# Performance work log

Measured on AMD Instinct MI355X. Metric: run time of the kernel, lower is better.

Reference implementation:

```python
import jax, jax.numpy as jnp
import numpy as np

B, V, K = 4, 16384, 16
E, F, D, H, L, ITERS = 32, 2, 64, 4, 2, 10
NEG = -1e9


def setup_inputs() -> dict:
    key = jax.random.key(0)
    ks = jax.random.split(key, 24)
    def g(k, shape, fan_in):
        return jax.random.normal(k, shape, dtype=jnp.float32) * (fan_in ** -0.5)
    inp = {}
    inp["node_embeddings"] = jax.random.normal(ks[0], (B, V, E), dtype=jnp.float32)
    inp["node_features"] = jax.random.normal(ks[1], (B, V, F), dtype=jnp.float32)
    inp["demands"] = jax.random.normal(ks[2], (B, V, 1), dtype=jnp.float32)
    # padded adjacency list; value == V means masked (no neighbor)
    inp["adj_lst"] = jax.random.randint(ks[3], (B, V, K), 0, V + 1, dtype=jnp.int32)
    # precomputed inverse-adjacency indices; reference computes inflow by scatter-add instead
    inp["flow_indices"] = jax.random.randint(ks[4], (B, V, K), 0, V, dtype=jnp.int32)
    inp["num_nodes"] = V
    din = E + F
    inp["W_enc1"] = g(ks[5], (din, D), din); inp["b_enc1"] = jnp.zeros((D,), jnp.float32)
    inp["W_enc2"] = g(ks[6], (D, D), D); inp["b_enc2"] = jnp.zeros((D,), jnp.float32)
    inp["W_gat"] = g(ks[7], (H, D, D), D)
    inp["a_src"] = g(ks[8], (H, D), D)
    inp["a_dst"] = g(ks[9], (H, D), D)
    for i, nm in enumerate(["z", "r", "c"]):
        inp["W_" + nm] = g(ks[10 + 2 * i], (D, D), D)
        inp["U_" + nm] = g(ks[11 + 2 * i], (D, D), D)
        inp["b_" + nm] = jnp.zeros((D,), jnp.float32)
    inp["W_dec1"] = g(ks[16], (D, D), D); inp["b_dec1"] = jnp.zeros((D,), jnp.float32)
    inp["W_dec2"] = g(ks[17], (D, 1), D); inp["b_dec2"] = jnp.zeros((1,), jnp.float32)
    return inp


def _forward(node_embeddings, node_features, demands,
             W_enc1, b_enc1, W_enc2, b_enc2,
             W_gat, a_src, a_dst,
             W_z, U_z, b_z, W_r, U_r, b_r, W_c, U_c, b_c,
             W_dec1, b_dec1, W_dec2, b_dec2,
             adj_lst, num_nodes):
    Vn = num_nodes
    bidx = jnp.arange(adj_lst.shape[0])[:, None, None]  # [B,1,1]
    mask = adj_lst == Vn  # [B,V,K] padded slots

    # --- node encoder MLP (tanh, activate_final=True) ---
    x = jnp.concatenate([node_embeddings, node_features], axis=-1)
    h = jnp.tanh(x @ W_enc1 + b_enc1)
    h = jnp.tanh(h @ W_enc2 + b_enc2)

    def gather_nodes(t):
        # masked_gather: pad with a zero row so index == num_nodes reads zeros
        t_pad = jnp.concatenate([t, jnp.zeros_like(t[:, :1])], axis=1)  # [B,V+1,Dt]
        return t_pad[bidx, adj_lst]  # [B,V,K,Dt]

    # --- graph_layers x (AdjGAT + GRU) ---
    for _ in range(L):
        agg = 0.0
        for hd in range(H):
            t = h @ W_gat[hd]                       # [B,V,D]
            nb = gather_nodes(t)                    # [B,V,K,D]
            scores = (t @ a_src[hd])[:, :, None] + nb @ a_dst[hd]  # [B,V,K]
            attn = jax.nn.softmax(jnp.where(mask, NEG, scores), axis=-1)
            agg = agg + jnp.einsum('bvk,bvkd->bvd', attn, nb)
        m = jnp.tanh(agg / H)
        z = jax.nn.sigmoid(m @ W_z + h @ U_z + b_z)
        r = jax.nn.sigmoid(m @ W_r + h @ U_r + b_r)
        c = jnp.tanh(m @ W_c + (r * h) @ U_c + b_c)
        h = (1.0 - z) * h + z * c

    # --- decoder -> per-edge weights via masked gather + softmax ---
    node_w = jnp.tanh(h @ W_dec1 + b_dec1) @ W_dec2 + b_dec2   # [B,V,1]
    pw = gather_nodes(node_w)[..., 0]                          # [B,V,K]
    norm_w = jax.nn.softmax(jnp.where(mask, NEG, pw), axis=-1)

    # --- iterative min-cost-flow solver ---
    flow0 = norm_w * jax.nn.relu(-demands)  # sources (demand<0) push supply
    def body(carry, _):
        flow, _ = carry
        inflow = jnp.zeros((flow.shape[0], Vn + 1), flow.dtype)
        inflow = inflow.at[bidx, adj_lst].add(flow)[:, :Vn]    # [B,V]
        new = norm_w * jax.nn.relu(inflow[..., None] - demands)
        return (new, flow), None
    (flow, pflow), _ = jax.lax.scan(body, (flow0, flow0), None, length=ITERS)

    flow_cost = jnp.sum(flow * flow, axis=(1, 2))  # quadratic cost_fn
    return flow, flow_cost, norm_w, pflow


def reference(node_embeddings, node_features, demands, adj_lst, flow_indices, num_nodes,
              W_enc1, b_enc1, W_enc2, b_enc2, W_gat, a_src, a_dst,
              W_z, U_z, b_z, W_r, U_r, b_r, W_c, U_c, b_c,
              W_dec1, b_dec1, W_dec2, b_dec2):
    # flow_indices is the precomputed inverse adjacency; inflow is computed
    # equivalently here by scatter-add over adj_lst.
    return _forward(node_embeddings, node_features, demands,
                    W_enc1, b_enc1, W_enc2, b_enc2,
                    W_gat, a_src, a_dst,
                    W_z, U_z, b_z, W_r, U_r, b_r, W_c, U_c, b_c,
                    W_dec1, b_dec1, W_dec2, b_dec2,
                    adj_lst, num_nodes)
```

## Files before the change

kernel.cpp:

```cpp
#include <hip/hip_runtime.h>
#include <stdint.h>
#include <math.h>

#define BN 4
#define VN 16384
#define KN 16
#define HN 4
#define NN (BN*VN)
#define EN (VN*KN)
#define CAP 64
#define NEGC (-1.0e9f)

typedef __attribute__((ext_vector_type(8))) short short8;
typedef __attribute__((ext_vector_type(4))) float floatx4;
typedef __attribute__((ext_vector_type(2))) float floatx2;
typedef unsigned short u16;
typedef unsigned int u32;

#define OFF_H      0ull
#define OFF_M      8388608ull
#define OFF_T      16777216ull
#define OFF_SS     50331648ull
#define OFF_NW     52428800ull
#define OFF_NV     52690944ull
#define OFF_CNT    53215232ull
#define OFF_PG     53477376ull
#define OFF_PZR    (OFF_PG  + 32768ull)
#define OFF_PC     (OFF_PZR + 32768ull)
#define OFF_PE1    (OFF_PC  + 16384ull)
#define OFF_PE2    (OFF_PE1 + 8192ull)
#define OFF_PD1    (OFF_PE2 + 8192ull)
#define OFF_PAV    (OFF_PD1 + 8192ull)

__device__ __forceinline__ u16 f2bf(float x){
  union { float f; unsigned int u; } c; c.f = x;
  unsigned int r = c.u + 0x7fffu + ((c.u >> 16) & 1u);
  return (u16)(r >> 16);
}
__device__ __forceinline__ float bf2f(u32 s){
  union { unsigned int u; float f; } c; c.u = s << 16;
  return c.f;
}
__device__ __forceinline__ float sigm(float x){ return 1.0f/(1.0f+expf(-x)); }

union S8 { short8 v; u16 u[8]; };

__global__ __launch_bounds__(256) void k_pack(
    const float* __restrict__ Wg,  const float* __restrict__ Wz, const float* __restrict__ Uz,
    const float* __restrict__ Wr,  const float* __restrict__ Ur, const float* __restrict__ Wc,
    const float* __restrict__ Uc,  const float* __restrict__ We1, const float* __restrict__ We2,
    const float* __restrict__ Wd1, const float* __restrict__ asrc, const float* __restrict__ adst,
    u16* __restrict__ pg, u16* __restrict__ pzr, u16* __restrict__ pc,
    u16* __restrict__ pe1, u16* __restrict__ pe2, u16* __restrict__ pd1,
    u16* __restrict__ pav)
{
  int e = blockIdx.x*256 + threadIdx.x;
  if (e >= 54272) return;
  int el; u16* dst; int CN; int region;
  if      (e < 16384){ el = e;        dst = pg;  CN = 2; region = 0; }
  else if (e < 32768){ el = e-16384;  dst = pzr; CN = 4; region = 1; }
  else if (e < 40960){ el = e-32768;  dst = pc;  CN = 4; region = 2; }
  else if (e < 45056){ el = e-40960;  dst = pe1; CN = 2; region = 3; }
  else if (e < 49152){ el = e-45056;  dst = pe2; CN = 2; region = 4; }
  else if (e < 53248){ el = e-49152;  dst = pd1; CN = 2; region = 5; }
  else               { el = e-53248;  dst = pav; CN = 2; region = 6; }
  int j    = el & 7;
  int lane = (el >> 3) & 63;
  int rest = el >> 9;
  int c  = rest % CN;
  int ng = rest / CN;
  int k  = c*32 + (lane>>4)*8 + j;
  int n  = ng*16 + (lane&15);
  float val = 0.0f;
  if (region == 0){
    val = Wg[(size_t)(n>>6)*4096 + k*64 + (n&63)];
  } else if (region == 1){
    int km = (k&3)*16 + ((k>>2)&15);
    if (n < 64) val = (k<64) ? Wz[km*64+n]      : Uz[(k-64)*64+n];
    else        val = (k<64) ? Wr[km*64+(n-64)] : Ur[(k-64)*64+(n-64)];
  } else if (region == 2){
    int km = (k&3)*16 + ((k>>2)&15);
    val = (k<64) ? Wc[km*64+n] : Uc[(k-64)*64+n];
  } else if (region == 3){
    val = (k<34) ? We1[k*64+n] : 0.0f;
  } else if (region == 4){
    val = We2[k*64+n];
  } else if (region == 5){
    val = Wd1[k*64+n];
  } else {
    int hd = (n>>1)&3, s = n&1;
    const float* av = s ? (adst + hd*64) : (asrc + hd*64);
    const float* wrow = Wg + (size_t)hd*4096 + k*64;
    float acc = 0.f;
    #pragma unroll 8
    for (int d=0; d<64; d++) acc += wrow[d]*av[d];
    val = acc;
  }
  dst[el] = f2bf(val);
}

template<int CN>
__device__ __forceinline__ void load_b(const u16* p, int chunk, int lane, short8 Bf[CN][4]){
  const short8* P = (const short8*)p;
  #pragma unroll
  for (int c=0;c<CN;c++)
    #pragma unroll
    for (int ng=0; ng<4; ng++)
      Bf[c][ng] = P[((chunk*4+ng)*CN + c)*64 + lane];
}

template<int CN>
__device__ __forceinline__ void mfma_tile(const short8* A, const short8 Bf[CN][4],
                                          floatx4 acc[4][4], int wave, int lane){
  #pragma unroll
  for (int c=0;c<CN;c++){
    #pragma unroll
    for (int mg=0;mg<4;mg++){
      short8 a = A[((wave*4+mg)*CN + c)*64 + lane];
      #pragma unroll
      for (int ng=0;ng<4;ng++)
        acc[mg][ng] = __builtin_amdgcn_mfma_f32_16x16x32_bf16(a, Bf[c][ng], acc[mg][ng], 0, 0, 0);
    }
  }
}

__device__ __forceinline__ void zero_acc(floatx4 acc[4][4]){
  #pragma unroll
  for (int mg=0;mg<4;mg++)
    #pragma unroll
    for (int ng=0;ng<4;ng++){
      floatx4 z = {0.f,0.f,0.f,0.f};
      acc[mg][ng] = z;
    }
}

__global__ __launch_bounds__(128) void k_enc(
    const float* __restrict__ emb, const float* __restrict__ feat,
    const u16* __restrict__ pe1, const u16* __restrict__ pe2,
    const float* __restrict__ be1, const float* __restrict__ be2,
    u16* __restrict__ hout, u32* __restrict__ cnt)
{
  cnt[blockIdx.x*128 + threadIdx.x] = 0u;
  __shared__ short8 A1[1024];
  __shared__ short8 A2[1024];
  const int tid = threadIdx.x;
  const int n0  = blockIdx.x * 128;
  for (int it=0; it<8; ++it){
    int slot = it*128 + tid;
    int row = slot >> 3, jc = slot & 7;
    S8 w;
    if (jc < 4){
      const float* s = emb + (size_t)(n0+row)*32 + jc*8;
      #pragma unroll
      for (int j=0;j<8;j++) w.u[j] = f2bf(s[j]);
    } else if (jc == 4){
      const float* s = feat + (size_t)(n0+row)*2;
      w.u[0] = f2bf(s[0]); w.u[1] = f2bf(s[1]);
      #pragma unroll
      for (int j=2;j<8;j++) w.u[j] = 0;
    } else {
      #pragma unroll
      for (int j=0;j<8;j++) w.u[j] = 0;
    }
    A1[((row>>4)*2 + (jc>>2))*64 + (jc&3)*16 + (row&15)] = w.v;
  }
  __syncthreads();
  const int wave = tid>>6, lane = tid&63, q = lane>>4, ml = lane&15;

  short8 Bf[2][4];
  load_b<2>(pe1, 0, lane, Bf);
  floatx4 acc[4][4];
  zero_acc(acc);
  mfma_tile<2>(A1, Bf, acc, wave, lane);

  u16* A2s = (u16*)A2;
  #pragma unroll
  for (int mg=0;mg<4;mg++){
    #pragma unroll
    for (int r=0;r<4;r++){
      int row_l = wave*64 + mg*16 + q*4 + r;
      #pragma unroll
      for (int ng=0;ng<4;ng++){
        int k2 = ng*16 + ml;
        float v = tanhf(acc[mg][ng][r] + be1[k2]);
        int c2 = k2>>5, q2=(k2>>3)&3, j2=k2&7;
        A2s[ (((row_l>>4)*2 + c2)*64 + q2*16 + (row_l&15))*8 + j2 ] = f2bf(v);
      }
    }
  }
  __syncthreads();

  load_b<2>(pe2, 0, lane, Bf);
  zero_acc(acc);
  mfma_tile<2>(A2, Bf, acc, wave, lane);
  #pragma unroll
  for (int mg=0;mg<4;mg++)
    #pragma unroll
    for (int r=0;r<4;r++){
      int row = n0 + wave*64 + mg*16 + q*4 + r;
      #pragma unroll
      for (int ng=0;ng<4;ng++){
        int col = ng*16 + ml;
        hout[(size_t)row*64 + col] = f2bf(tanhf(acc[mg][ng][r] + be2[col]));
      }
    }
}

__global__ __launch_bounds__(128) void k_t(
    const u16* __restrict__ h, const u16* __restrict__ pg, const u16* __restrict__ pav,
    u32* __restrict__ tq, float* __restrict__ ss)
{
  __shared__ short8 A[1024];
  const int tid = threadIdx.x;
  const int n0  = blockIdx.x * 128;
  const short8* hp = (const short8*)h;
  for (int it=0; it<8; ++it){
    int slot = it*128 + tid;
    int row = slot >> 3, jc = slot & 7;
    A[((row>>4)*2 + (jc>>2))*64 + (jc&3)*16 + (row&15)] = hp[(size_t)(n0+row)*8 + jc];
  }
  __syncthreads();
  const int wave = tid>>6, lane = tid&63, q = lane>>4, ml = lane&15;

  for (int chunk=0; chunk<4; ++chunk){
    short8 Bf[2][4];
    load_b<2>(pg, chunk, lane, Bf);
    floatx4 acc[4][4];
    zero_acc(acc);
    mfma_tile<2>(A, Bf, acc, wave, lane);

    #pragma unroll
    for (int mg=0;mg<4;mg++){
      #pragma unroll
      for (int r=0;r<4;r++){
        int row = n0 + wave*64 + mg*16 + q*4 + r;
        int pk = __builtin_amdgcn_cvt_pk_fp8_f32(acc[mg][0][r], acc[mg][1][r], 0, false);
        pk     = __builtin_amdgcn_cvt_pk_fp8_f32(acc[mg][2][r], acc[mg][3][r], pk, true);
        tq[(size_t)row*64 + chunk*16 + ml] = (u32)pk;
      }
    }
  }

  const short8* Pv = (const short8*)pav;
  short8 Bs0 = Pv[lane], Bs1 = Pv[64 + lane];
  #pragma unroll
  for (int mg=0;mg<4;mg++){
    floatx4 sacc = {0.f,0.f,0.f,0.f};
    short8 a0 = A[((wave*4+mg)*2 + 0)*64 + lane];
    short8 a1 = A[((wave*4+mg)*2 + 1)*64 + lane];
    sacc = __builtin_amdgcn_mfma_f32_16x16x32_bf16(a0, Bs0, sacc, 0, 0, 0);
    sacc = __builtin_amdgcn_mfma_f32_16x16x32_bf16(a1, Bs1, sacc, 0, 0, 0);
    if (ml < 8){
      #pragma unroll
      for (int r=0;r<4;r++){
        int row = n0 + wave*64 + mg*16 + q*4 + r;
        ss[(size_t)row*8 + ml] = sacc[r];
      }
    }
  }
}

__global__ __launch_bounds__(256) void k_attn(
    const int* __restrict__ adj, const u32* __restrict__ tq,
    const float* __restrict__ ss, u16* __restrict__ m)
{
  const int wave = threadIdx.x>>6, lane = threadIdx.x&63;
  const int nid = blockIdx.x*4 + wave;
  const int b = nid >> 14;
  const int hd = lane>>4;
  int u = adj[(size_t)nid*16 + (lane&15)];
  float sc = (u == VN) ? NEGC : (ss[(size_t)nid*8 + hd*2] + ss[((size_t)b*VN + u)*8 + hd*2 + 1]);
  float mx = sc;
  #pragma unroll
  for (int s=1;s<16;s<<=1) mx = fmaxf(mx, __shfl_xor(mx, s, 64));
  float ex = expf(sc - mx);
  float sm = ex;
  #pragma unroll
  for (int s=1;s<16;s<<=1) sm += __shfl_xor(sm, s, 64);
  float attn = ex / sm;

  float a0=0.f, a1=0.f, a2=0.f, a3=0.f;
  const int srcl = lane & 48;
  #pragma unroll
  for (int k2=0;k2<16;k2++){
    int u2 = __shfl(u, k2, 64);
    float av = __shfl(attn, srcl + k2, 64);
    u32 w = tq[((size_t)b*VN + u2)*64 + lane];
    floatx2 f01 = __builtin_amdgcn_cvt_pk_f32_fp8((int)w, false);
    floatx2 f23 = __builtin_amdgcn_cvt_pk_f32_fp8((int)w, true);
    a0 += av*f01.x; a1 += av*f01.y; a2 += av*f23.x; a3 += av*f23.y;
  }
  a0 += __shfl_xor(a0,16,64); a0 += __shfl_xor(a0,32,64);
  a1 += __shfl_xor(a1,16,64); a1 += __shfl_xor(a1,32,64);
  a2 += __shfl_xor(a2,16,64); a2 += __shfl_xor(a2,32,64);
  a3 += __shfl_xor(a3,16,64); a3 += __shfl_xor(a3,32,64);
  if (lane < 16){
    union { uint2 v; u16 u[4]; } val;
    val.u[0] = f2bf(tanhf(a0*0.25f)); val.u[1] = f2bf(tanhf(a1*0.25f));
    val.u[2] = f2bf(tanhf(a2*0.25f)); val.u[3] = f2bf(tanhf(a3*0.25f));
    *(uint2*)(m + (size_t)nid*64 + lane*4) = val.v;
  }
}

__global__ __launch_bounds__(128) void k_gru(
    const u16* __restrict__ m, u16* __restrict__ h,
    const u16* __restrict__ pzr, const u16* __restrict__ pc_,
    const float* __restrict__ bz, const float* __restrict__ br,
    const float* __restrict__ bc_)
{
  __shared__ short8 A[2048];
  const int tid = threadIdx.x;
  const int n0  = blockIdx.x * 128;
  const short8* mp = (const short8*)m;
  const short8* hp = (const short8*)h;
  for (int it=0; it<16; ++it){
    int slot = it*128 + tid;
    int row = slot >> 4, jc = slot & 15;
    short8 w = (jc < 8) ? mp[(size_t)(n0+row)*8 + jc]
                        : hp[(size_t)(n0+row)*8 + (jc-8)];
    A[((row>>4)*4 + (jc>>2))*64 + (jc&3)*16 + (row&15)] = w;
  }
  __syncthreads();
  const int wave = tid>>6, lane = tid&63, q = lane>>4, ml = lane&15;

  short8 Bf[4][4];

  floatx4 zacc[4][4];
  load_b<4>(pzr, 0, lane, Bf);
  zero_acc(zacc);
  mfma_tile<4>(A, Bf, zacc, wave, lane);

  floatx4 acc[4][4];
  load_b<4>(pzr, 1, lane, Bf);
  zero_acc(acc);
  mfma_tile<4>(A, Bf, acc, wave, lane);

  floatx4 h_old[4][4];
  u16* As = (u16*)A;
  #pragma unroll
  for (int mg=0;mg<4;mg++){
    #pragma unroll
    for (int r=0;r<4;r++){
      int row_l = wave*64 + mg*16 + q*4 + r;
      int row   = n0 + row_l;
      #pragma unroll
      for (int ng=0;ng<4;ng++){
        int col = ng*16 + ml;
        float rv = sigm(acc[mg][ng][r] + br[col]);
        float hv = bf2f(h[(size_t)row*64 + col]);
        h_old[mg][ng][r] = hv;
        int kk = 64 + col;
        int c2 = kk>>5, q2 = (kk>>3)&3, j2 = kk&7;
        As[ (((row_l>>4)*4 + c2)*64 + q2*16 + (row_l&15))*8 + j2 ] = f2bf(hv*rv);
      }
    }
  }

  load_b<4>(pc_, 0, lane, Bf);
  zero_acc(acc);
  mfma_tile<4>(A, Bf, acc, wave, lane);

  #pragma unroll
  for (int mg=0;mg<4;mg++)
    #pragma unroll
    for (int r=0;r<4;r++){
      int row = n0 + wave*64 + mg*16 + q*4 + r;
      #pragma unroll
      for (int ng=0;ng<4;ng++){
        int col = ng*16 + ml;
        float zv = sigm(zacc[mg][ng][r] + bz[col]);
        float cv = tanhf(acc[mg][ng][r] + bc_[col]);
        float ho = h_old[mg][ng][r];
        h[(size_t)row*64 + col] = f2bf((1.f - zv)*ho + zv*cv);
      }
    }
}

__global__ __launch_bounds__(128) void k_dec(
    const u16* __restrict__ h, const u16* __restrict__ pd1,
    const float* __restrict__ bd1, const float* __restrict__ Wd2, const float* __restrict__ bd2,
    float* __restrict__ nodew, float* __restrict__ cost)
{
  {
    int t = blockIdx.x*128 + threadIdx.x;
    if (t < BN) cost[t] = 0.f;
  }
  __shared__ short8 A[1024];
  const int tid = threadIdx.x;
  const int n0  = blockIdx.x * 128;
  const short8* hp = (const short8*)h;
  for (int it=0; it<8; ++it){
    int slot = it*128 + tid;
    int row = slot >> 3, jc = slot & 7;
    A[((row>>4)*2 + (jc>>2))*64 + (jc&3)*16 + (row&15)] = hp[(size_t)(n0+row)*8 + jc];
  }
  __syncthreads();
  const int wave = tid>>6, lane = tid&63, q = lane>>4, ml = lane&15;

  short8 Bf[2][4];
  load_b<2>(pd1, 0, lane, Bf);
  floatx4 acc[4][4];
  zero_acc(acc);
  mfma_tile<2>(A, Bf, acc, wave, lane);

  float wd2l[4];
  #pragma unroll
  for (int ng=0;ng<4;ng++) wd2l[ng] = Wd2[ng*16 + ml];
  float b2 = bd2[0];
  #pragma unroll
  for (int mg=0;mg<4;mg++)
    #pragma unroll
    for (int r=0;r<4;r++){
      int row = n0 + wave*64 + mg*16 + q*4 + r;
      float ps = 0.f;
      #pragma unroll
      for (int ng=0;ng<4;ng++)
        ps += tanhf(acc[mg][ng][r] + bd1[ng*16+ml]) * wd2l[ng];
      #pragma unroll
      for (int s=1;s<16;s<<=1) ps += __shfl_xor(ps, s, 64);
      if (ml == 0) nodew[row] = ps + b2;
    }
}

__global__ __launch_bounds__(256) void k_pw(
    const int* __restrict__ adj, const float* __restrict__ nodew, const float* __restrict__ dem,
    float* __restrict__ normw, float* __restrict__ nv0,
    u32* __restrict__ cnt, u32* __restrict__ bucket)
{
  int e = blockIdx.x*256 + threadIdx.x;
  int node = e >> 4;
  int b = node >> 14;
  int u = adj[e];
  float pw = (u == VN) ? NEGC : nodew[(size_t)b*VN + u];
  float mx = pw;
  #pragma unroll
  for (int s=1;s<16;s<<=1) mx = fmaxf(mx, __shfl_xor(mx, s, 64));
  float ex = expf(pw - mx);
  float sm = ex;
  #pragma unroll
  for (int s=1;s<16;s<<=1) sm += __shfl_xor(sm, s, 64);
  float nw = ex / sm;
  normw[e] = nw;
  if ((e & 15) == 0) nv0[node] = fmaxf(-dem[node], 0.f);
  if (u < VN){
    int g = b*VN + u;
    u32 pos = atomicAdd(&cnt[g], 1u);
    if (pos < CAP)
      bucket[(size_t)g*CAP + pos] = ((u32)f2bf(nw) << 16) | (u32)(node & (VN-1));
  }
}

__global__ __launch_bounds__(256) void k_gather(
    const u32* __restrict__ cnt, const u32* __restrict__ bucket,
    const float* __restrict__ dem, const float* __restrict__ nvin, float* __restrict__ nvout,
    const float* __restrict__ normw, float* __restrict__ fout, float* __restrict__ cost)
{
  int tid = blockIdx.x*256 + threadIdx.x;
  int g = tid >> 4;
  int lane = tid & 15;
  int b = g >> 14;
  u32 n = cnt[g];
  if (n > CAP) n = CAP;
  const u32* bk = bucket + (size_t)g*CAP;
  const float* nb = nvin + (size_t)b*VN;
  float sum = 0.f;
  for (u32 i = (u32)lane; i < n; i += 16u){
    u32 r = bk[i];
    sum += bf2f(r >> 16) * nb[r & 0xFFFFu];
  }
  #pragma unroll
  for (int sh=1; sh<16; sh<<=1) sum += __shfl_xor(sum, sh, 64);
  float nvv = fmaxf(sum - dem[g], 0.f);
  if (lane == 0) nvout[g] = nvv;
  if (fout){
    int e = g*16 + lane;
    float fl = normw[e] * nvv;
    fout[e] = fl;
    if (cost){
      float ssq = fl*fl;
      #pragma unroll
      for (int sh=1; sh<64; sh<<=1) ssq += __shfl_xor(ssq, sh, 64);
      __shared__ float part[4];
      if ((threadIdx.x & 63) == 0) part[threadIdx.x>>6] = ssq;
      __syncthreads();
      if (threadIdx.x == 0) atomicAdd(cost + b, part[0]+part[1]+part[2]+part[3]);
    }
  }
}

extern "C" void kernel_launch(void* const* d_in, const int* in_sizes, int n_in,
                              void* d_out, int out_size, void* d_ws, size_t ws_size,
                              hipStream_t stream)
{
  const float* emb  = (const float*)d_in[0];
  const float* feat = (const float*)d_in[1];
  const float* dem  = (const float*)d_in[2];
  const int*   adj  = (const int*)  d_in[3];
  const float* We1 = (const float*)d_in[6];
  const float* be1 = (const float*)d_in[7];
  const float* We2 = (const float*)d_in[8];
  const float* be2 = (const float*)d_in[9];
  const float* Wg  = (const float*)d_in[10];
  const float* asrc= (const float*)d_in[11];
  const float* adst= (const float*)d_in[12];
  const float* Wz  = (const float*)d_in[13];
  const float* Uz  = (const float*)d_in[14];
  const float* bz  = (const float*)d_in[15];
  const float* Wr  = (const float*)d_in[16];
  const float* Ur  = (const float*)d_in[17];
  const float* br  = (const float*)d_in[18];
  const float* Wc  = (const float*)d_in[19];
  const float* Uc  = (const float*)d_in[20];
  const float* bc  = (const float*)d_in[21];
  const float* Wd1 = (const float*)d_in[22];
  const float* bd1 = (const float*)d_in[23];
  const float* Wd2 = (const float*)d_in[24];
  const float* bd2 = (const float*)d_in[25];

  char* ws = (char*)d_ws;
  u16*   h     = (u16*)  (ws + OFF_H);
  u16*   m     = (u16*)  (ws + OFF_M);
  u32*   tq    = (u32*)  (ws + OFF_T);
  u32*   bucket= (u32*)  (ws + OFF_T);
  float* ss    = (float*)(ws + OFF_SS);
  float* nodew = (float*)(ws + OFF_NW);
  float* nv    = (float*)(ws + OFF_NV);
  u32*   cnt   = (u32*)  (ws + OFF_CNT);
  u16* pg  = (u16*)(ws + OFF_PG);
  u16* pzr = (u16*)(ws + OFF_PZR);
  u16* pc  = (u16*)(ws + OFF_PC);
  u16* pe1 = (u16*)(ws + OFF_PE1);
  u16* pe2 = (u16*)(ws + OFF_PE2);
  u16* pd1 = (u16*)(ws + OFF_PD1);
  u16* pav = (u16*)(ws + OFF_PAV);
  float* nv0b = nv;
  float* nv1b = nv + NN;

  float* out0 = (float*)d_out;
  float* out1 = out0 + 1048576;
  float* out2 = out0 + 1048580;
  float* out3 = out0 + 2097156;

  k_pack<<<212, 256, 0, stream>>>(Wg, Wz, Uz, Wr, Ur, Wc, Uc, We1, We2, Wd1,
                                  asrc, adst, pg, pzr, pc, pe1, pe2, pd1, pav);
  k_enc<<<512, 128, 0, stream>>>(emb, feat, pe1, pe2, be1, be2, h, cnt);

  for (int l=0; l<2; ++l){
    k_t   <<<512, 128, 0, stream>>>(h, pg, pav, tq, ss);
    k_attn<<<16384, 256, 0, stream>>>(adj, tq, ss, m);
    k_gru <<<512, 128, 0, stream>>>(m, h, pzr, pc, bz, br, bc);
  }

  k_dec<<<512, 128, 0, stream>>>(h, pd1, bd1, Wd2, bd2, nodew, out1);
  k_pw <<<4096, 256, 0, stream>>>(adj, nodew, dem, out2, nv0b, cnt, bucket);

  for (int i=1; i<=10; ++i){
    float* in  = (i & 1) ? nv0b : nv1b;
    float* out = (i & 1) ? nv1b : nv0b;
    float* fo  = (i==10) ? out0 : ((i==9) ? out3 : nullptr);
    k_gather<<<4096, 256, 0, stream>>>(cnt, bucket, dem, in, out, out2, fo,
                                       (i==10) ? out1 : nullptr);
  }
}
```

Measured before the change: 461.9 us.

## Fuse decoder MLP into final GRU layer and remap blocks by batch for locality

On the last layer, the GRU kernel now keeps the new hidden state in shared memory, runs the decoder MLP there and writes node weights directly. This removes the separate decoder kernel and the hidden-state round trip through global memory. The attn, pw and gather kernels also remap block indices so that consecutive blocks are spread across the batches in an interleaved pattern, which is meant to improve L2 and XCD locality for the per-batch random gathers. The cost-zeroing moves into k_pw. The final hidden state is no longer written back to global memory.

Result: faster. 444.6 us, median of 3 (-3.8%).

```diff
diff --git a/kernel.cpp b/kernel.cpp
--- a/kernel.cpp
+++ b/kernel.cpp
@@ -265,8 +265,10 @@
     const float* __restrict__ ss, u16* __restrict__ m)
 {
   const int wave = threadIdx.x>>6, lane = threadIdx.x&63;
-  const int nid = blockIdx.x*4 + wave;
-  const int b = nid >> 14;
+  const int bid = blockIdx.x;
+  const int b   = (bid & 7) >> 1;
+  const int loc = (bid >> 3)*2 + (bid & 1);
+  const int nid = b*VN + loc*4 + wave;
   const int hd = lane>>4;
   int u = adj[(size_t)nid*16 + (lane&15)];
   float sc = (u == VN) ? NEGC : (ss[(size_t)nid*8 + hd*2] + ss[((size_t)b*VN + u)*8 + hd*2 + 1]);
@@ -306,7 +308,10 @@
     const u16* __restrict__ m, u16* __restrict__ h,
     const u16* __restrict__ pzr, const u16* __restrict__ pc_,
     const float* __restrict__ bz, const float* __restrict__ br,
-    const float* __restrict__ bc_)
+    const float* __restrict__ bc_,
+    const u16* __restrict__ pd1, const float* __restrict__ bd1,
+    const float* __restrict__ Wd2, const float* __restrict__ bd2,
+    float* __restrict__ nodew)
 {
   __shared__ short8 A[2048];
   const int tid = threadIdx.x;
@@ -364,72 +369,71 @@
   for (int mg=0;mg<4;mg++)
     #pragma unroll
     for (int r=0;r<4;r++){
-      int row = n0 + wave*64 + mg*16 + q*4 + r;
+      int row_l = wave*64 + mg*16 + q*4 + r;
+      int row   = n0 + row_l;
       #pragma unroll
       for (int ng=0;ng<4;ng++){
         int col = ng*16 + ml;
         float zv = sigm(zacc[mg][ng][r] + bz[col]);
         float cv = tanhf(acc[mg][ng][r] + bc_[col]);
         float ho = h_old[mg][ng][r];
-        h[(size_t)row*64 + col] = f2bf((1.f - zv)*ho + zv*cv);
-      }
-    }
-}
-
-__global__ __launch_bounds__(128) void k_dec(
-    const u16* __restrict__ h, const u16* __restrict__ pd1,
-    const float* __restrict__ bd1, const float* __restrict__ Wd2, const float* __restrict__ bd2,
-    float* __restrict__ nodew, float* __restrict__ cost)
-{
-  {
-    int t = blockIdx.x*128 + threadIdx.x;
-    if (t < BN) cost[t] = 0.f;
-  }
-  __shared__ short8 A[1024];
-  const int tid = threadIdx.x;
-  const int n0  = blockIdx.x * 128;
-  const short8* hp = (const short8*)h;
-  for (int it=0; it<8; ++it){
-    int slot = it*128 + tid;
-    int row = slot >> 3, jc = slot & 7;
-    A[((row>>4)*2 + (jc>>2))*64 + (jc&3)*16 + (row&15)] = hp[(size_t)(n0+row)*8 + jc];
-  }
-  __syncthreads();
-  const int wave = tid>>6, lane = tid&63, q = lane>>4, ml = lane&15;
-
-  short8 Bf[2][4];
-  load_b<2>(pd1, 0, lane, Bf);
-  floatx4 acc[4][4];
-  zero_acc(acc);
-  mfma_tile<2>(A, Bf, acc, wave, lane);
-
-  float wd2l[4];
-  #pragma unroll
-  for (int ng=0;ng<4;ng++) wd2l[ng] = Wd2[ng*16 + ml];
-  float b2 = bd2[0];
-  #pragma unroll
-  for (int mg=0;mg<4;mg++)
-    #pragma unroll
-    for (int r=0;r<4;r++){
-      int row = n0 + wave*64 + mg*16 + q*4 + r;
-      float ps = 0.f;
-      #pragma unroll
-      for (int ng=0;ng<4;ng++)
-        ps += tanhf(acc[mg][ng][r] + bd1[ng*16+ml]) * wd2l[ng];
-      #pragma unroll
-      for (int s=1;s<16;s<<=1) ps += __shfl_xor(ps, s, 64);
-      if (ml == 0) nodew[row] = ps + b2;
-    }
+        float hn = (1.f - zv)*ho + zv*cv;
+        if (nodew == nullptr){
+          h[(size_t)row*64 + col] = f2bf(hn);
+        } else {
+          int kk = 64 + col;
+          int c2 = kk>>5, q2 = (kk>>3)&3, j2 = kk&7;
+          As[ (((row_l>>4)*4 + c2)*64 + q2*16 + (row_l&15))*8 + j2 ] = f2bf(hn);
+        }
+      }
+    }
+
+  if (nodew){
+    short8 Bd[2][4];
+    load_b<2>(pd1, 0, lane, Bd);
+    floatx4 dacc[4][4];
+    zero_acc(dacc);
+    #pragma unroll
+    for (int c=0;c<2;c++){
+      #pragma unroll
+      for (int mg=0;mg<4;mg++){
+        short8 a = A[((wave*4+mg)*4 + (2+c))*64 + lane];
+        #pragma unroll
+        for (int ng=0;ng<4;ng++)
+          dacc[mg][ng] = __builtin_amdgcn_mfma_f32_16x16x32_bf16(a, Bd[c][ng], dacc[mg][ng], 0, 0, 0);
+      }
+    }
+    float wd2l[4];
+    #pragma unroll
+    for (int ng=0;ng<4;ng++) wd2l[ng] = Wd2[ng*16 + ml];
+    float b2 = bd2[0];
+    #pragma unroll
+    for (int mg=0;mg<4;mg++)
+      #pragma unroll
+      for (int r=0;r<4;r++){
+        int row = n0 + wave*64 + mg*16 + q*4 + r;
+        float ps = 0.f;
+        #pragma unroll
+        for (int ng=0;ng<4;ng++)
+          ps += tanhf(dacc[mg][ng][r] + bd1[ng*16+ml]) * wd2l[ng];
+        #pragma unroll
+        for (int s=1;s<16;s<<=1) ps += __shfl_xor(ps, s, 64);
+        if (ml == 0) nodew[row] = ps + b2;
+      }
+  }
 }
 
 __global__ __launch_bounds__(256) void k_pw(
     const int* __restrict__ adj, const float* __restrict__ nodew, const float* __restrict__ dem,
     float* __restrict__ normw, float* __restrict__ nv0,
-    u32* __restrict__ cnt, u32* __restrict__ bucket)
-{
-  int e = blockIdx.x*256 + threadIdx.x;
-  int node = e >> 4;
-  int b = node >> 14;
+    u32* __restrict__ cnt, u32* __restrict__ bucket, float* __restrict__ cost)
+{
+  if (blockIdx.x == 0 && threadIdx.x < BN) cost[threadIdx.x] = 0.f;
+  const int bid = blockIdx.x;
+  const int b   = (bid & 7) >> 1;
+  const int loc = (bid >> 3)*2 + (bid & 1);
+  int node = b*VN + loc*16 + (threadIdx.x >> 4);
+  int e = node*16 + (threadIdx.x & 15);
   int u = adj[e];
   float pw = (u == VN) ? NEGC : nodew[(size_t)b*VN + u];
   float mx = pw;
@@ -455,10 +459,11 @@
     const float* __restrict__ dem, const float* __restrict__ nvin, float* __restrict__ nvout,
     const float* __restrict__ normw, float* __restrict__ fout, float* __restrict__ cost)
 {
-  int tid = blockIdx.x*256 + threadIdx.x;
-  int g = tid >> 4;
-  int lane = tid & 15;
-  int b = g >> 14;
+  const int bid = blockIdx.x;
+  const int b   = (bid & 7) >> 1;
+  const int loc = (bid >> 3)*2 + (bid & 1);
+  int g = b*VN + loc*16 + (threadIdx.x >> 4);
+  int lane = threadIdx.x & 15;
   u32 n = cnt[g];
   if (n > CAP) n = CAP;
   const u32* bk = bucket + (size_t)g*CAP;
@@ -548,11 +553,11 @@
   for (int l=0; l<2; ++l){
     k_t   <<<512, 128, 0, stream>>>(h, pg, pav, tq, ss);
     k_attn<<<16384, 256, 0, stream>>>(adj, tq, ss, m);
-    k_gru <<<512, 128, 0, stream>>>(m, h, pzr, pc, bz, br, bc);
-  }
-
-  k_dec<<<512, 128, 0, stream>>>(h, pd1, bd1, Wd2, bd2, nodew, out1);
-  k_pw <<<4096, 256, 0, stream>>>(adj, nodew, dem, out2, nv0b, cnt, bucket);
+    k_gru <<<512, 128, 0, stream>>>(m, h, pzr, pc, bz, br, bc,
+                                    pd1, bd1, Wd2, bd2, (l==1) ? nodew : nullptr);
+  }
+
+  k_pw <<<4096, 256, 0, stream>>>(adj, nodew, dem, out2, nv0b, cnt, bucket, out1);
 
   for (int i=1; i<=10; ++i){
     float* in  = (i & 1) ? nv0b : nv1b;
```
